# Kernel optimization log

Measured on AMD Instinct MI355X. Metric: run time of the kernel, lower is better.

Reference implementation:

```python
import jax, jax.numpy as jnp
import numpy as np

EPS = 1e-6

def elu_feature_map(x):
    return jax.nn.elu(x) + 1.0

def setup_inputs() -> dict:
    key = jax.random.key(0)
    ks = jax.random.split(key, 5)
    B, S, D, H, Hd = 4, 4096, 1024, 16, 64
    scale = 1.0 / np.sqrt(D)
    x = jax.random.normal(ks[0], (B, S, D), dtype=jnp.float32)
    Wq = jax.random.normal(ks[1], (D, H, Hd), dtype=jnp.float32) * scale
    Wk = jax.random.normal(ks[2], (D, H, Hd), dtype=jnp.float32) * scale
    Wv = jax.random.normal(ks[3], (D, H, Hd), dtype=jnp.float32) * scale
    Wo = jax.random.normal(ks[4], (H, Hd, D), dtype=jnp.float32) * (1.0 / np.sqrt(H * Hd))
    bq = jnp.zeros((H, Hd), dtype=jnp.float32)
    bk = jnp.zeros((H, Hd), dtype=jnp.float32)
    bv = jnp.zeros((H, Hd), dtype=jnp.float32)
    bo = jnp.zeros((D,), dtype=jnp.float32)
    return {"x": x, "Wq": Wq, "bq": bq, "Wk": Wk, "bk": bk, "Wv": Wv, "bv": bv, "Wo": Wo, "bo": bo}

def reference(x, Wq, bq, Wk, bk, Wv, bv, Wo, bo):
    # QKV projections: [n,s,D] x [D,h,d] -> [n,s,h,d]
    q = jnp.einsum('nsD,Dhd->nshd', x, Wq) + bq
    k = jnp.einsum('nsD,Dhd->nshd', x, Wk) + bk
    v = jnp.einsum('nsD,Dhd->nshd', x, Wv) + bv
    qf = elu_feature_map(q)
    kf = elu_feature_map(k)
    # kv state per head: [n,h,m,d]
    kv = jnp.einsum('nshd,nshm->nhmd', kf, v)
    # normalizer: [n,l,h]
    z = 1.0 / (jnp.einsum('nlhd,nhd->nlh', qf, jnp.sum(kf, axis=1)) + EPS)
    # output: [n,l,h,m]
    y = jnp.einsum('nlhd,nhmd,nlh->nlhm', qf, kv, z)
    # output projection contracting (head, head_dim)
    out = jnp.einsum('nlhm,hmD->nlD', y, Wo) + bo
    return out
```

## Files before the change

kernel.cpp:

```cpp
#include <hip/hip_runtime.h>
#include <cstddef>
#include <cstdint>


typedef __attribute__((ext_vector_type(8))) __bf16 bf16x8;
typedef __attribute__((ext_vector_type(4))) __bf16 bf16x4;
typedef __attribute__((ext_vector_type(2))) __bf16 bf16x2;
typedef __attribute__((ext_vector_type(4))) float f32x4;

__device__ __forceinline__ void async_cp16(const void* g, void* s) {
    __builtin_amdgcn_global_load_lds(
        (__attribute__((address_space(1))) void*)g,
        (__attribute__((address_space(3))) void*)s, 16, 0, 0);
}


#define QUAD(ARR, BRR, RO, CO)                                                 \
    _Pragma("unroll")                                                          \
    for (int _qi = 0; _qi < 4; ++_qi)                                          \
        _Pragma("unroll")                                                      \
        for (int _qj = 0; _qj < 2; ++_qj)                                      \
            _Pragma("unroll")                                                  \
            for (int _qk = 0; _qk < 2; ++_qk)                                  \
                acc[(RO) + _qi][(CO) + _qj] =                                  \
                    __builtin_amdgcn_mfma_f32_16x16x32_bf16(                   \
                        ARR[_qi][_qk], BRR[_qj][_qk],                          \
                        acc[(RO) + _qi][(CO) + _qj], 0, 0, 0);

__device__ __forceinline__ void mfma256_core(const __bf16* __restrict__ A,
                                             const __bf16* __restrict__ BT,
                                             int mbase, int nbase,
                                             f32x4 acc[8][4])
{
    extern __shared__ __bf16 lds[];
    const int t    = threadIdx.x;
    const int lane = t & 63;
    const int wid  = t >> 6;
    const int wm   = wid >> 2;
    const int wn   = wid & 3;
    const int fr   = lane & 15;
    const int fq   = lane >> 4;
    const int srow  = lane >> 3;
    const int sslot = ((lane & 7) ^ srow) << 3;

    const __bf16* aBase = A  + (size_t)mbase * 1024;
    const __bf16* bBase = BT + (size_t)nbase * 1024;

#define STAGE_AH(tile, hh, bb)                                                 \
    { _Pragma("unroll") for (int _i = 0; _i < 2; ++_i) {                       \
          const int _c = 2 * wid + _i;                                         \
          async_cp16(aBase + (size_t)((hh) * 128 + _c * 8 + srow) * 1024       \
                         + (tile) * 64 + sslot,                                \
                     lds + (bb) * 32768 + (hh) * 8192 + _c * 512); } }
#define STAGE_BH(tile, hh, bb)                                                 \
    { _Pragma("unroll") for (int _i = 0; _i < 2; ++_i) {                       \
          const int _c = 2 * wid + _i;                                         \
          async_cp16(bBase + (size_t)((hh) * 128 + _c * 8 + srow) * 1024       \
                         + (tile) * 64 + sslot,                                \
                     lds + (bb) * 32768 + 16384 + (hh) * 8192 + _c * 512); } }
#define LDA(ri, ks, b)                                                         \
    (*(const bf16x8*)(lds + (b) * 32768 + (wm * 128 + (ri) * 16 + fr) * 64     \
                      + (((ks) * 32 + fq * 8) ^ ((fr & 7) << 3))))
#define LDB(cj, ks, b)                                                         \
    (*(const bf16x8*)(lds + (b) * 32768 + 16384                                \
                      + (wn * 64 + (cj) * 16 + fr) * 64                        \
                      + (((ks) * 32 + fq * 8) ^ ((fr & 7) << 3))))

#define PHASE_END                                                              \
    asm volatile("s_waitcnt lgkmcnt(0)" ::: "memory");                         \
    __builtin_amdgcn_s_barrier();

#define KTILE(T, BC, BN, S2, NX, P2W)                                          \
    {                                                                          \
                                                             \
        _Pragma("unroll") for (int _i = 0; _i < 4; ++_i) {                     \
            aR1[_i][0] = LDA(4 + _i, 0, BC);                                   \
            aR1[_i][1] = LDA(4 + _i, 1, BC);                                   \
        }                                                                      \
        _Pragma("unroll") for (int _j = 0; _j < 2; ++_j) {                     \
            bC1[_j][0] = LDB(2 + _j, 0, BC);                                   \
            bC1[_j][1] = LDB(2 + _j, 1, BC);                                   \
        }                                                                      \
        if (NX) STAGE_BH((T) + 1, 1, BN)                                       \
        __builtin_amdgcn_sched_barrier(0);                                     \
        __builtin_amdgcn_s_setprio(1);                                         \
        QUAD(aR0, bC0, 0, 0)                                                   \
        __builtin_amdgcn_s_setprio(0);                                         \
        PHASE_END                                                              \
                                                             \
        if (NX) asm volatile("s_waitcnt vmcnt(4)" ::: "memory");               \
        if (S2) STAGE_AH((T) + 2, 0, BC)                                       \
        __builtin_amdgcn_sched_barrier(0);                                     \
        __builtin_amdgcn_s_setprio(1);                                         \
        QUAD(aR0, bC1, 0, 2)                                                   \
        __builtin_amdgcn_s_setprio(0);                                         \
        PHASE_END                                                              \
                                                             \
        if (NX) asm volatile("s_waitcnt vmcnt(" P2W ")" ::: "memory");         \
        if (NX) {                                                              \
            _Pragma("unroll") for (int _i = 0; _i < 4; ++_i) {                 \
                aR0[_i][0] = LDA(_i, 0, BN);                                   \
                aR0[_i][1] = LDA(_i, 1, BN);                                   \
            }                                                                  \
        }                                                                      \
        if (S2) STAGE_AH((T) + 2, 1, BC)                                       \
        __builtin_amdgcn_sched_barrier(0);                                     \
        __builtin_amdgcn_s_setprio(1);                                         \
        QUAD(aR1, bC0, 4, 0)                                                   \
        __builtin_amdgcn_s_setprio(0);                                         \
        PHASE_END                                                              \
                                                             \
        if (NX) {                                                              \
            _Pragma("unroll") for (int _j = 0; _j < 2; ++_j) {                 \
                bC0[_j][0] = LDB(_j, 0, BN);                                   \
                bC0[_j][1] = LDB(_j, 1, BN);                                   \
            }                                                                  \
        }                                                                      \
        if (S2) STAGE_BH((T) + 2, 0, BC)                                       \
        __builtin_amdgcn_sched_barrier(0);                                     \
        __builtin_amdgcn_s_setprio(1);                                         \
        QUAD(aR1, bC1, 4, 2)                                                   \
        __builtin_amdgcn_s_setprio(0);                                         \
        PHASE_END                                                              \
    }

    bf16x8 aR0[4][2], aR1[4][2], bC0[2][2], bC1[2][2];

    STAGE_AH(0, 0, 0) STAGE_AH(0, 1, 0) STAGE_BH(0, 0, 0) STAGE_BH(0, 1, 0)
    STAGE_AH(1, 0, 1) STAGE_AH(1, 1, 1) STAGE_BH(1, 0, 1)
    asm volatile("s_waitcnt vmcnt(6)" ::: "memory");
    __builtin_amdgcn_s_barrier();

#pragma unroll
    for (int i = 0; i < 4; ++i) {
        aR0[i][0] = LDA(i, 0, 0);
        aR0[i][1] = LDA(i, 1, 0);
    }
#pragma unroll
    for (int j = 0; j < 2; ++j) {
        bC0[j][0] = LDB(j, 0, 0);
        bC0[j][1] = LDB(j, 1, 0);
    }

    for (int T = 0; T < 14; ++T) {
        const int bc = T & 1, bn = bc ^ 1;
        KTILE(T, bc, bn, 1, 1, "2")
    }
    KTILE(14, 0, 1, 0, 1, "0")
    KTILE(15, 1, 0, 0, 0, "0")

#undef KTILE
#undef PHASE_END
#undef STAGE_AH
#undef STAGE_BH
#undef LDA
#undef LDB
}

__global__ __launch_bounds__(512) void gemm_qkv_256(
    const __bf16* __restrict__ xb,
    const __bf16* __restrict__ wqt, const __bf16* __restrict__ wkt,
    const __bf16* __restrict__ wvt,
    const float* __restrict__ bq, const float* __restrict__ bk,
    const float* __restrict__ bv,
    __bf16* __restrict__ qfb, __bf16* __restrict__ kfb, __bf16* __restrict__ vb)
{
    f32x4 acc[8][4];
#pragma unroll
    for (int i = 0; i < 8; ++i)
#pragma unroll
        for (int j = 0; j < 4; ++j) acc[i][j] = (f32x4){0.f, 0.f, 0.f, 0.f};

    const int o   = blockIdx.x;
    const int swz = (o & 7) * 96 + (o >> 3);
    const int mt  = swz / 12;
    const int ntl = swz - mt * 12;

    const int which = ntl >> 2;
    const int nbase = (ntl & 3) * 256;
    const int mbase = mt * 256;

    const __bf16* BT  = (which == 0) ? wqt : (which == 1) ? wkt : wvt;
    const float* bias = (which == 0) ? bq : (which == 1) ? bk : bv;
    __bf16* outp      = (which == 0) ? qfb : (which == 1) ? kfb : vb;
    const bool feat   = (which < 2);

    mfma256_core(xb, BT, mbase, nbase, acc);

    const int t = threadIdx.x, lane = t & 63, wid = t >> 6;
    const int wm = wid >> 2, wn = wid & 3;
    const int fr = lane & 15, fq = lane >> 4;

#pragma unroll
    for (int ri = 0; ri < 8; ++ri)
#pragma unroll
        for (int cj = 0; cj < 4; ++cj) {
            const int col = nbase + wn * 64 + cj * 16 + fr;
            const float bval = bias[col];
#pragma unroll
            for (int r = 0; r < 4; ++r) {
                const int row = mbase + wm * 128 + ri * 16 + fq * 4 + r;
                float vv = acc[ri][cj][r] + bval;
                if (feat) vv = (vv > 0.f) ? (vv + 1.f) : __expf(vv);
                outp[(size_t)row * 1024 + col] = (__bf16)vv;
            }
        }
}

__global__ __launch_bounds__(512) void gemm_out_256(
    const __bf16* __restrict__ yb, const __bf16* __restrict__ wot,
    const float* __restrict__ bo, float* __restrict__ out)
{
    f32x4 acc[8][4];
#pragma unroll
    for (int i = 0; i < 8; ++i)
#pragma unroll
        for (int j = 0; j < 4; ++j) acc[i][j] = (f32x4){0.f, 0.f, 0.f, 0.f};

    const int o   = blockIdx.x;
    const int swz = (o & 7) * 32 + (o >> 3);
    const int mbase = (swz >> 2) * 256;
    const int nbase = (swz & 3) * 256;

    mfma256_core(yb, wot, mbase, nbase, acc);

    const int t = threadIdx.x, lane = t & 63, wid = t >> 6;
    const int wm = wid >> 2, wn = wid & 3;
    const int fr = lane & 15, fq = lane >> 4;

#pragma unroll
    for (int ri = 0; ri < 8; ++ri)
#pragma unroll
        for (int cj = 0; cj < 4; ++cj) {
            const int col = nbase + wn * 64 + cj * 16 + fr;
            const float bval = bo[col];
#pragma unroll
            for (int r = 0; r < 4; ++r) {
                const int row = mbase + wm * 128 + ri * 16 + fq * 4 + r;
                out[(size_t)row * 1024 + col] = acc[ri][cj][r] + bval;
            }
        }
}

__global__ __launch_bounds__(256) void kv_ksum_mfma(
    const __bf16* __restrict__ kfb, const __bf16* __restrict__ vb,
    float* __restrict__ kvp, float* __restrict__ ksp)
{
    __shared__ __bf16 kfs[64 * 66];
    __shared__ __bf16 vs[64 * 66];

    const int bh = blockIdx.x;
    const int n = bh >> 4, h = bh & 15;
    const int chunk = blockIdx.y;
    const int t = threadIdx.x, lane = t & 63, w = t >> 6;
    const int fr = lane & 15, fq = lane >> 4;

    f32x4 acc[4];
#pragma unroll
    for (int j = 0; j < 4; j++) acc[j] = (f32x4){0.f, 0.f, 0.f, 0.f};
    f32x4 accks = (f32x4){0.f, 0.f, 0.f, 0.f};

    bf16x8 ones;
#pragma unroll
    for (int e = 0; e < 8; e++) ones[e] = (__bf16)1.0f;

    const size_t base = ((size_t)n * 4096 + (size_t)chunk * 256) * 1024 + h * 64;

    for (int tile = 0; tile < 4; tile++) {
#pragma unroll
        for (int i = 0; i < 2; i++) {
            int idx = t + i * 256;
            int s = idx >> 3, d0 = (idx & 7) * 8;
            bf16x8 k8 = *(const bf16x8*)(kfb + base + (size_t)(tile * 64 + s) * 1024 + d0);
            bf16x8 v8 = *(const bf16x8*)(vb  + base + (size_t)(tile * 64 + s) * 1024 + d0);
#pragma unroll
            for (int e = 0; e < 4; e++) {
                *(bf16x2*)(kfs + s * 66 + d0 + 2 * e) = (bf16x2){k8[2*e], k8[2*e+1]};
                *(bf16x2*)(vs  + s * 66 + d0 + 2 * e) = (bf16x2){v8[2*e], v8[2*e+1]};
            }
        }
        __syncthreads();

#pragma unroll
        for (int kk = 0; kk < 2; kk++) {
            bf16x8 af, bfr[4];
#pragma unroll
            for (int j = 0; j < 8; j++)
                af[j] = vs[(kk * 32 + fq * 8 + j) * 66 + 16 * w + fr];
#pragma unroll
            for (int j2 = 0; j2 < 4; j2++)
#pragma unroll
                for (int j = 0; j < 8; j++)
                    bfr[j2][j] = kfs[(kk * 32 + fq * 8 + j) * 66 + 16 * j2 + fr];
#pragma unroll
            for (int j2 = 0; j2 < 4; j2++)
                acc[j2] = __builtin_amdgcn_mfma_f32_16x16x32_bf16(
                    af, bfr[j2], acc[j2], 0, 0, 0);
            accks = __builtin_amdgcn_mfma_f32_16x16x32_bf16(
                ones, bfr[w], accks, 0, 0, 0);
        }
        __syncthreads();
    }

    const size_t pbase = ((size_t)bh * 16 + chunk) * 4096;
#pragma unroll
    for (int j2 = 0; j2 < 4; j2++)
#pragma unroll
        for (int r = 0; r < 4; r++) {
            int m = 16 * w + fq * 4 + r;
            int d = 16 * j2 + fr;
            kvp[pbase + m * 64 + d] = acc[j2][r];
        }
    if (fq == 0)
        ksp[((size_t)bh * 16 + chunk) * 64 + 16 * w + fr] = accks[0];
}

__global__ __launch_bounds__(256) void reduce_kv(
    const float* __restrict__ kvp, const float* __restrict__ ksp,
    __bf16* __restrict__ kvb, __bf16* __restrict__ ksumb)
{
    const int b = blockIdx.x;
    if (b < 1024) {
        int i = b * 256 + threadIdx.x;
        int bh = i >> 12, md = i & 4095;
        float s = 0.f;
#pragma unroll
        for (int c = 0; c < 16; c++) s += kvp[((size_t)bh * 16 + c) * 4096 + md];
        kvb[i] = (__bf16)s;
    } else {
        int j = (b - 1024) * 256 + threadIdx.x;
        int bh = j >> 6, d = j & 63;
        float s = 0.f;
#pragma unroll
        for (int c = 0; c < 16; c++) s += ksp[((size_t)bh * 16 + c) * 64 + d];
        ksumb[j] = (__bf16)s;
    }
}

__global__ __launch_bounds__(256) void y_mfma(
    const __bf16* __restrict__ qfb, const __bf16* __restrict__ kvb,
    const __bf16* __restrict__ ksumb, __bf16* __restrict__ yb)
{
    __shared__ __bf16 qs[128 * 72];
    __shared__ __bf16 kvs[64 * 72];

    const int gbase = blockIdx.x * 128;
    const int h = blockIdx.y;
    const int bh = (gbase >> 12) * 16 + h;
    const int t = threadIdx.x, lane = t & 63, w = t >> 6;
    const int fr = lane & 15, fq = lane >> 4;

#pragma unroll
    for (int i = 0; i < 4; i++) {
        int idx = t + i * 256;
        int l = idx >> 3, d0 = (idx & 7) * 8;
        *(bf16x8*)(qs + l * 72 + d0) =
            *(const bf16x8*)(qfb + (size_t)(gbase + l) * 1024 + h * 64 + d0);
    }
#pragma unroll
    for (int i = 0; i < 2; i++) {
        int idx = t + i * 256;
        int m = idx >> 3, d0 = (idx & 7) * 8;
        *(bf16x8*)(kvs + m * 72 + d0) =
            *(const bf16x8*)(kvb + (size_t)bh * 4096 + m * 64 + d0);
    }
    bf16x8 ksb[2];
#pragma unroll
    for (int kk = 0; kk < 2; kk++)
        ksb[kk] = *(const bf16x8*)(ksumb + bh * 64 + kk * 32 + fq * 8);
    __syncthreads();

    f32x4 acc[2][4], accz[2];
#pragma unroll
    for (int i = 0; i < 2; i++) {
        accz[i] = (f32x4){0.f, 0.f, 0.f, 0.f};
#pragma unroll
        for (int j = 0; j < 4; j++) acc[i][j] = (f32x4){0.f, 0.f, 0.f, 0.f};
    }

#pragma unroll
    for (int kk = 0; kk < 2; kk++) {
        bf16x8 af[2], bfr[4];
#pragma unroll
        for (int i = 0; i < 2; i++)
            af[i] = *(const bf16x8*)(qs + (32 * w + 16 * i + fr) * 72 + kk * 32 + fq * 8);
#pragma unroll
        for (int j = 0; j < 4; j++)
            bfr[j] = *(const bf16x8*)(kvs + (16 * j + fr) * 72 + kk * 32 + fq * 8);
#pragma unroll
        for (int i = 0; i < 2; i++) {
#pragma unroll
            for (int j = 0; j < 4; j++)
                acc[i][j] = __builtin_amdgcn_mfma_f32_16x16x32_bf16(
                    af[i], bfr[j], acc[i][j], 0, 0, 0);
            accz[i] = __builtin_amdgcn_mfma_f32_16x16x32_bf16(
                af[i], ksb[kk], accz[i], 0, 0, 0);
        }
    }

#pragma unroll
    for (int i = 0; i < 2; i++)
#pragma unroll
        for (int r = 0; r < 4; r++) {
            const float z = 1.0f / (accz[i][r] + 1e-6f);
            const int g = gbase + 32 * w + 16 * i + fq * 4 + r;
#pragma unroll
            for (int j = 0; j < 4; j++)
                yb[(size_t)g * 1024 + h * 64 + 16 * j + fr] =
                    (__bf16)(acc[i][j][r] * z);
        }
}

__global__ __launch_bounds__(256) void prep(
    const float* __restrict__ x, __bf16* __restrict__ xb,
    const float* __restrict__ w0, const float* __restrict__ w1,
    const float* __restrict__ w2, const float* __restrict__ w3,
    __bf16* __restrict__ o0, __bf16* __restrict__ o1,
    __bf16* __restrict__ o2, __bf16* __restrict__ o3)
{
    __shared__ float ld[32][33];
    const int b = blockIdx.x;
    const int t = threadIdx.x;

    if (b < 8192) {
        const size_t i = ((size_t)b * 256 + t) * 8;
        float4 a = *(const float4*)(x + i);
        float4 c = *(const float4*)(x + i + 4);
        bf16x8 o;
        o[0] = (__bf16)a.x; o[1] = (__bf16)a.y; o[2] = (__bf16)a.z; o[3] = (__bf16)a.w;
        o[4] = (__bf16)c.x; o[5] = (__bf16)c.y; o[6] = (__bf16)c.z; o[7] = (__bf16)c.w;
        *(bf16x8*)(xb + i) = o;
        return;
    }

    const int idx  = b - 8192;
    const int wsel = idx >> 10;
    const int yy   = (idx >> 5) & 31;
    const int xx   = idx & 31;
    const float* src = (wsel == 0) ? w0 : (wsel == 1) ? w1 : (wsel == 2) ? w2 : w3;
    __bf16* dst      = (wsel == 0) ? o0 : (wsel == 1) ? o1 : (wsel == 2) ? o2 : o3;

    const int kbase = xx * 32;
    const int nbase = yy * 32;
    const int r = t >> 3, c4 = (t & 7) * 4;

    float4 a = *(const float4*)(src + (size_t)(kbase + r) * 1024 + nbase + c4);
    ld[r][c4 + 0] = a.x; ld[r][c4 + 1] = a.y; ld[r][c4 + 2] = a.z; ld[r][c4 + 3] = a.w;
    __syncthreads();

    bf16x4 o;
    o[0] = (__bf16)ld[c4 + 0][r];
    o[1] = (__bf16)ld[c4 + 1][r];
    o[2] = (__bf16)ld[c4 + 2][r];
    o[3] = (__bf16)ld[c4 + 3][r];
    *(bf16x4*)(dst + (size_t)(nbase + r) * 1024 + kbase + c4) = o;
}

extern "C" void kernel_launch(void* const* d_in, const int* in_sizes, int n_in,
                              void* d_out, int out_size, void* d_ws, size_t ws_size,
                              hipStream_t stream)
{
    const float* x  = (const float*)d_in[0];
    const float* Wq = (const float*)d_in[1];
    const float* bq = (const float*)d_in[2];
    const float* Wk = (const float*)d_in[3];
    const float* bk = (const float*)d_in[4];
    const float* Wv = (const float*)d_in[5];
    const float* bv = (const float*)d_in[6];
    const float* Wo = (const float*)d_in[7];
    const float* bo = (const float*)d_in[8];
    float* out = (float*)d_out;

    __bf16* xb    = (__bf16*)d_ws;
    __bf16* wqt   = xb + (size_t)16777216;
    __bf16* wkt   = wqt + 1048576;
    __bf16* wvt   = wkt + 1048576;
    __bf16* wot   = wvt + 1048576;
    __bf16* qfb   = wot + 1048576;
    __bf16* kfb   = qfb + (size_t)16777216;
    __bf16* vb    = kfb + (size_t)16777216;
    float*  kvp   = (float*)(vb + (size_t)16777216);
    float*  ksp   = kvp + 4194304;
    __bf16* kvb   = (__bf16*)(ksp + 65536);
    __bf16* ksumb = kvb + 262144;

    const int LDS_BYTES = 131072;
    (void)hipFuncSetAttribute((const void*)gemm_qkv_256,
                              hipFuncAttributeMaxDynamicSharedMemorySize, LDS_BYTES);
    (void)hipFuncSetAttribute((const void*)gemm_out_256,
                              hipFuncAttributeMaxDynamicSharedMemorySize, LDS_BYTES);

    prep<<<dim3(12288), dim3(256), 0, stream>>>(
        x, xb, Wq, Wk, Wv, Wo, wqt, wkt, wvt, wot);

    gemm_qkv_256<<<dim3(768), dim3(512), LDS_BYTES, stream>>>(
        xb, wqt, wkt, wvt, bq, bk, bv, qfb, kfb, vb);
    kv_ksum_mfma<<<dim3(64, 16), dim3(256), 0, stream>>>(kfb, vb, kvp, ksp);
    reduce_kv<<<dim3(1040), dim3(256), 0, stream>>>(kvp, ksp, kvb, ksumb);
    y_mfma<<<dim3(128, 16), dim3(256), 0, stream>>>(qfb, kvb, ksumb, kfb);
    gemm_out_256<<<dim3(256), dim3(512), LDS_BYTES, stream>>>(kfb, wot, bo, out);
}
```

Before: 327.0 us.

## Fuse per-head y computation into output projection GEMM

Replaces the separate y_mfma kernel and the output GEMM with a single kernel. For each head, the kernel computes the normalized y tile in LDS from qf, kv and ksum, then feeds it straight into the output-projection MFMA accumulation. This drops the global write and re-read of the 32 MB y buffer and one launch. The cost is that the new per-head loop loads synchronously with vmcnt(0) and full barriers and has no double buffering, so it loses the pipelined load/compute overlap the old GEMM core had. Each output tile also recomputes y for its 256 rows, once for each of the 4 column blocks.

```diff
diff --git a/kernel.cpp b/kernel.cpp
--- a/kernel.cpp
+++ b/kernel.cpp
@@ -13,6 +13,9 @@
         (__attribute__((address_space(1))) void*)g,
         (__attribute__((address_space(3))) void*)s, 16, 0, 0);
 }
+
+#define MFMA16(d, a, b) \
+    d = __builtin_amdgcn_mfma_f32_16x16x32_bf16(a, b, d, 0, 0, 0)
 
 
 #define QUAD(ARR, BRR, RO, CO)                                                 \
@@ -72,7 +75,6 @@
 
 #define KTILE(T, BC, BN, S2, NX, P2W)                                          \
     {                                                                          \
-                                                             \
         _Pragma("unroll") for (int _i = 0; _i < 4; ++_i) {                     \
             aR1[_i][0] = LDA(4 + _i, 0, BC);                                   \
             aR1[_i][1] = LDA(4 + _i, 1, BC);                                   \
@@ -87,7 +89,6 @@
         QUAD(aR0, bC0, 0, 0)                                                   \
         __builtin_amdgcn_s_setprio(0);                                         \
         PHASE_END                                                              \
-                                                             \
         if (NX) asm volatile("s_waitcnt vmcnt(4)" ::: "memory");               \
         if (S2) STAGE_AH((T) + 2, 0, BC)                                       \
         __builtin_amdgcn_sched_barrier(0);                                     \
@@ -95,7 +96,6 @@
         QUAD(aR0, bC1, 0, 2)                                                   \
         __builtin_amdgcn_s_setprio(0);                                         \
         PHASE_END                                                              \
-                                                             \
         if (NX) asm volatile("s_waitcnt vmcnt(" P2W ")" ::: "memory");         \
         if (NX) {                                                              \
             _Pragma("unroll") for (int _i = 0; _i < 4; ++_i) {                 \
@@ -109,7 +109,6 @@
         QUAD(aR1, bC0, 4, 0)                                                   \
         __builtin_amdgcn_s_setprio(0);                                         \
         PHASE_END                                                              \
-                                                             \
         if (NX) {                                                              \
             _Pragma("unroll") for (int _j = 0; _j < 2; ++_j) {                 \
                 bC0[_j][0] = LDB(_j, 0, BN);                                   \
@@ -207,26 +206,127 @@
         }
 }
 
-__global__ __launch_bounds__(512) void gemm_out_256(
-    const __bf16* __restrict__ yb, const __bf16* __restrict__ wot,
+__global__ __launch_bounds__(512) void y_out_fused(
+    const __bf16* __restrict__ qfb, const __bf16* __restrict__ kvb,
+    const __bf16* __restrict__ ksumb, const __bf16* __restrict__ wot,
     const float* __restrict__ bo, float* __restrict__ out)
 {
-    f32x4 acc[8][4];
-#pragma unroll
-    for (int i = 0; i < 8; ++i)
-#pragma unroll
-        for (int j = 0; j < 4; ++j) acc[i][j] = (f32x4){0.f, 0.f, 0.f, 0.f};
+    extern __shared__ __bf16 lds[];
+    __bf16* bufQ  = lds;
+    __bf16* bufW  = lds + 16384;
+    __bf16* bufY  = lds + 32768;
+    __bf16* bufKV = lds + 49152;
+
+    const int t = threadIdx.x, lane = t & 63, wid = t >> 6;
+    const int wm = wid >> 2, wn = wid & 3;
+    const int fr = lane & 15, fq = lane >> 4;
+    const int srow  = lane >> 3;
+    const int sslot = ((lane & 7) ^ srow) << 3;
 
     const int o   = blockIdx.x;
     const int swz = (o & 7) * 32 + (o >> 3);
     const int mbase = (swz >> 2) * 256;
     const int nbase = (swz & 3) * 256;
-
-    mfma256_core(yb, wot, mbase, nbase, acc);
-
-    const int t = threadIdx.x, lane = t & 63, wid = t >> 6;
-    const int wm = wid >> 2, wn = wid & 3;
-    const int fr = lane & 15, fq = lane >> 4;
+    const int batch16 = (mbase >> 12) * 16;
+
+    const __bf16* qBase = qfb + (size_t)mbase * 1024;
+    const __bf16* wBase = wot + (size_t)nbase * 1024;
+
+    f32x4 acc[8][4];
+#pragma unroll
+    for (int i = 0; i < 8; ++i)
+#pragma unroll
+        for (int j = 0; j < 4; ++j) acc[i][j] = (f32x4){0.f, 0.f, 0.f, 0.f};
+
+    for (int h = 0; h < 16; ++h) {
+        const int bh = batch16 + h;
+
+        __syncthreads();
+
+#pragma unroll
+        for (int hh = 0; hh < 2; ++hh)
+#pragma unroll
+            for (int i2 = 0; i2 < 2; ++i2) {
+                const int c = 2 * wid + i2;
+                async_cp16(qBase + (size_t)(hh * 128 + c * 8 + srow) * 1024
+                               + h * 64 + sslot,
+                           bufQ + hh * 8192 + c * 512);
+                async_cp16(wBase + (size_t)(hh * 128 + c * 8 + srow) * 1024
+                               + h * 64 + sslot,
+                           bufW + hh * 8192 + c * 512);
+            }
+        {
+            const int kr = t >> 3, kc = t & 7;
+            async_cp16(kvb + (size_t)bh * 4096 + kr * 64
+                           + ((kc ^ (kr & 7)) << 3),
+                       bufKV + t * 8);
+        }
+        asm volatile("s_waitcnt vmcnt(0)" ::: "memory");
+        __syncthreads();
+
+        bf16x8 ksb[2];
+        ksb[0] = *(const bf16x8*)(ksumb + bh * 64 + fq * 8);
+        ksb[1] = *(const bf16x8*)(ksumb + bh * 64 + 32 + fq * 8);
+
+        f32x4 yac[2][4], zac[2];
+#pragma unroll
+        for (int i = 0; i < 2; ++i) {
+            zac[i] = (f32x4){0.f, 0.f, 0.f, 0.f};
+#pragma unroll
+            for (int j = 0; j < 4; ++j) yac[i][j] = (f32x4){0.f, 0.f, 0.f, 0.f};
+        }
+
+#pragma unroll
+        for (int kk = 0; kk < 2; ++kk) {
+            bf16x8 af[2], bkv[4];
+#pragma unroll
+            for (int i = 0; i < 2; ++i)
+                af[i] = *(const bf16x8*)(bufQ + (32 * wid + 16 * i + fr) * 64
+                             + ((kk * 32 + fq * 8) ^ ((fr & 7) << 3)));
+#pragma unroll
+            for (int j = 0; j < 4; ++j)
+                bkv[j] = *(const bf16x8*)(bufKV + (16 * j + fr) * 64
+                             + ((kk * 32 + fq * 8) ^ ((fr & 7) << 3)));
+#pragma unroll
+            for (int i = 0; i < 2; ++i) {
+#pragma unroll
+                for (int j = 0; j < 4; ++j) MFMA16(yac[i][j], af[i], bkv[j]);
+                MFMA16(zac[i], af[i], ksb[kk]);
+            }
+        }
+
+#pragma unroll
+        for (int i = 0; i < 2; ++i)
+#pragma unroll
+            for (int r = 0; r < 4; ++r) {
+                const int row = 32 * wid + 16 * i + fq * 4 + r;
+                const float z = 1.0f / (zac[i][r] + 1e-6f);
+#pragma unroll
+                for (int j = 0; j < 4; ++j) {
+                    const int col = 16 * j + fr;
+                    bufY[row * 64 + ((((col >> 3) ^ (row & 7)) << 3) | (col & 7))]
+                        = (__bf16)(yac[i][j][r] * z);
+                }
+            }
+        __syncthreads();
+
+#pragma unroll
+        for (int kk = 0; kk < 2; ++kk) {
+            bf16x8 ay[8], bw[4];
+#pragma unroll
+            for (int ri = 0; ri < 8; ++ri)
+                ay[ri] = *(const bf16x8*)(bufY + (wm * 128 + ri * 16 + fr) * 64
+                             + ((kk * 32 + fq * 8) ^ ((fr & 7) << 3)));
+#pragma unroll
+            for (int cj = 0; cj < 4; ++cj)
+                bw[cj] = *(const bf16x8*)(bufW + (wn * 64 + cj * 16 + fr) * 64
+                             + ((kk * 32 + fq * 8) ^ ((fr & 7) << 3)));
+#pragma unroll
+            for (int ri = 0; ri < 8; ++ri)
+#pragma unroll
+                for (int cj = 0; cj < 4; ++cj) MFMA16(acc[ri][cj], ay[ri], bw[cj]);
+        }
+    }
 
 #pragma unroll
     for (int ri = 0; ri < 8; ++ri)
@@ -335,80 +435,6 @@
         for (int c = 0; c < 16; c++) s += ksp[((size_t)bh * 16 + c) * 64 + d];
         ksumb[j] = (__bf16)s;
     }
-}
-
-__global__ __launch_bounds__(256) void y_mfma(
-    const __bf16* __restrict__ qfb, const __bf16* __restrict__ kvb,
-    const __bf16* __restrict__ ksumb, __bf16* __restrict__ yb)
-{
-    __shared__ __bf16 qs[128 * 72];
-    __shared__ __bf16 kvs[64 * 72];
-
-    const int gbase = blockIdx.x * 128;
-    const int h = blockIdx.y;
-    const int bh = (gbase >> 12) * 16 + h;
-    const int t = threadIdx.x, lane = t & 63, w = t >> 6;
-    const int fr = lane & 15, fq = lane >> 4;
-
-#pragma unroll
-    for (int i = 0; i < 4; i++) {
-        int idx = t + i * 256;
-        int l = idx >> 3, d0 = (idx & 7) * 8;
-        *(bf16x8*)(qs + l * 72 + d0) =
-            *(const bf16x8*)(qfb + (size_t)(gbase + l) * 1024 + h * 64 + d0);
-    }
-#pragma unroll
-    for (int i = 0; i < 2; i++) {
-        int idx = t + i * 256;
-        int m = idx >> 3, d0 = (idx & 7) * 8;
-        *(bf16x8*)(kvs + m * 72 + d0) =
-            *(const bf16x8*)(kvb + (size_t)bh * 4096 + m * 64 + d0);
-    }
-    bf16x8 ksb[2];
-#pragma unroll
-    for (int kk = 0; kk < 2; kk++)
-        ksb[kk] = *(const bf16x8*)(ksumb + bh * 64 + kk * 32 + fq * 8);
-    __syncthreads();
-
-    f32x4 acc[2][4], accz[2];
-#pragma unroll
-    for (int i = 0; i < 2; i++) {
-        accz[i] = (f32x4){0.f, 0.f, 0.f, 0.f};
-#pragma unroll
-        for (int j = 0; j < 4; j++) acc[i][j] = (f32x4){0.f, 0.f, 0.f, 0.f};
-    }
-
-#pragma unroll
-    for (int kk = 0; kk < 2; kk++) {
-        bf16x8 af[2], bfr[4];
-#pragma unroll
-        for (int i = 0; i < 2; i++)
-            af[i] = *(const bf16x8*)(qs + (32 * w + 16 * i + fr) * 72 + kk * 32 + fq * 8);
-#pragma unroll
-        for (int j = 0; j < 4; j++)
-            bfr[j] = *(const bf16x8*)(kvs + (16 * j + fr) * 72 + kk * 32 + fq * 8);
-#pragma unroll
-        for (int i = 0; i < 2; i++) {
-#pragma unroll
-            for (int j = 0; j < 4; j++)
-                acc[i][j] = __builtin_amdgcn_mfma_f32_16x16x32_bf16(
-                    af[i], bfr[j], acc[i][j], 0, 0, 0);
-            accz[i] = __builtin_amdgcn_mfma_f32_16x16x32_bf16(
-                af[i], ksb[kk], accz[i], 0, 0, 0);
-        }
-    }
-
-#pragma unroll
-    for (int i = 0; i < 2; i++)
-#pragma unroll
-        for (int r = 0; r < 4; r++) {
-            const float z = 1.0f / (accz[i][r] + 1e-6f);
-            const int g = gbase + 32 * w + 16 * i + fq * 4 + r;
-#pragma unroll
-            for (int j = 0; j < 4; j++)
-                yb[(size_t)g * 1024 + h * 64 + 16 * j + fr] =
-                    (__bf16)(acc[i][j][r] * z);
-        }
 }
 
 __global__ __launch_bounds__(256) void prep(
@@ -484,19 +510,20 @@
     __bf16* kvb   = (__bf16*)(ksp + 65536);
     __bf16* ksumb = kvb + 262144;
 
-    const int LDS_BYTES = 131072;
+    const int LDS_GEMM  = 131072;
+    const int LDS_FUSED = 106496;
     (void)hipFuncSetAttribute((const void*)gemm_qkv_256,
-                              hipFuncAttributeMaxDynamicSharedMemorySize, LDS_BYTES);
-    (void)hipFuncSetAttribute((const void*)gemm_out_256,
-                              hipFuncAttributeMaxDynamicSharedMemorySize, LDS_BYTES);
+                              hipFuncAttributeMaxDynamicSharedMemorySize, LDS_GEMM);
+    (void)hipFuncSetAttribute((const void*)y_out_fused,
+                              hipFuncAttributeMaxDynamicSharedMemorySize, LDS_FUSED);
 
     prep<<<dim3(12288), dim3(256), 0, stream>>>(
         x, xb, Wq, Wk, Wv, Wo, wqt, wkt, wvt, wot);
 
-    gemm_qkv_256<<<dim3(768), dim3(512), LDS_BYTES, stream>>>(
+    gemm_qkv_256<<<dim3(768), dim3(512), LDS_GEMM, stream>>>(
         xb, wqt, wkt, wvt, bq, bk, bv, qfb, kfb, vb);
     kv_ksum_mfma<<<dim3(64, 16), dim3(256), 0, stream>>>(kfb, vb, kvp, ksp);
     reduce_kv<<<dim3(1040), dim3(256), 0, stream>>>(kvp, ksp, kvb, ksumb);
-    y_mfma<<<dim3(128, 16), dim3(256), 0, stream>>>(qfb, kvb, ksumb, kfb);
-    gemm_out_256<<<dim3(256), dim3(512), LDS_BYTES, stream>>>(kfb, wot, bo, out);
-}
+    y_out_fused<<<dim3(256), dim3(512), LDS_FUSED, stream>>>(
+        qfb, kvb, ksumb, wot, bo, out);
+}
```

Result: slower. 350.6 us (+7.2%).
